# Performance work log

Hardware: AMD Instinct MI355X
Metric: run time of the kernel (lower is better)

## Reference

```python
import jax, jax.numpy as jnp
import numpy as np

EMB = 512
LIN = 64
ATT = 64
H = 8
EPS = 1e-6


def layer_norm(x, eps=EPS):
    # layer norm over last dim, no affine params (matches F.layer_norm w/o weight/bias)
    mu = jnp.mean(x, axis=-1, keepdims=True)
    var = jnp.var(x, axis=-1, keepdims=True)
    return (x - mu) * jax.lax.rsqrt(var + eps)


def setup_inputs() -> dict:
    key = jax.random.key(0)
    k1, k2, k3, k4, k5 = jax.random.split(key, 5)
    B, N = 8, 2048
    x = jax.random.normal(k1, (B, N, EMB), dtype=jnp.float32)
    rel_pos_bias = jax.random.normal(k2, (H, N, N), dtype=jnp.float32)
    invalid_attn_mask = jnp.ones((B, N, N), dtype=jnp.float32)
    uvqk = jax.random.normal(k3, (EMB, LIN * 2 * H + ATT * H * 2), dtype=jnp.float32) * 0.02
    o_w = jax.random.normal(k4, (EMB, LIN * H), dtype=jnp.float32) * (1.0 / np.sqrt(LIN * H))
    o_b = jnp.zeros((EMB,), dtype=jnp.float32)
    return {"x": x, "rel_pos_bias": rel_pos_bias, "invalid_attn_mask": invalid_attn_mask,
            "uvqk": uvqk, "o_w": o_w, "o_b": o_b}


def reference(x, rel_pos_bias, invalid_attn_mask, uvqk, o_w, o_b):
    B, N, D = x.shape
    residual = x
    normed = layer_norm(x)                                   # [B,N,D]
    proj = jax.nn.silu(jnp.einsum('bnd,de->bne', normed, uvqk))  # [B,N,2*LIN*H+2*ATT*H]
    lh = LIN * H
    ah = ATT * H
    u = proj[..., :lh]                                        # [B,N,LIN*H]
    v = proj[..., lh:2 * lh].reshape(B, N, H, LIN)            # [B,N,H,LIN]
    q = proj[..., 2 * lh:2 * lh + ah].reshape(B, N, H, ATT)
    k = proj[..., 2 * lh + ah:].reshape(B, N, H, ATT)
    qk = jnp.einsum('bnhd,bmhd->bhnm', q, k) + rel_pos_bias[None]  # [B,H,N,N]
    qk = jax.nn.silu(qk) * invalid_attn_mask[:, None]
    attn = jnp.einsum('bhnm,bmhd->bnhd', qk, v).reshape(B, N, lh)
    gated = u * layer_norm(attn)
    out = jnp.einsum('bnf,ef->bne', gated, o_w) + o_b          # dropout off (eval)
    return residual + out
```

## Files before the change

kernel.cpp:

```cpp
#include <hip/hip_runtime.h>
#include <stdint.h>

typedef short bf16x8   __attribute__((ext_vector_type(8)));
typedef short short4v  __attribute__((ext_vector_type(4)));
typedef short short8v  __attribute__((ext_vector_type(8)));
typedef float f32x4    __attribute__((ext_vector_type(4)));

typedef __attribute__((address_space(3))) uint32_t lds_u32;
typedef const __attribute__((address_space(1))) uint32_t glob_u32;

__device__ __forceinline__ void gl_lds16(const void* g, void* l) {
  __builtin_amdgcn_global_load_lds((glob_u32*)g, (lds_u32*)l, 16, 0, 0);
}

__device__ __forceinline__ float bf2f(short u) {
  union { float f; uint32_t i; } v; v.i = ((uint32_t)(uint16_t)u) << 16; return v.f;
}
__device__ __forceinline__ short f2bf(float f) {
  union { float f; uint32_t i; } v; v.f = f;
  uint32_t r = v.i + 0x7FFFu + ((v.i >> 16) & 1u);
  return (short)(r >> 16);
}
__device__ __forceinline__ float siluf(float x) {
  return x * __builtin_amdgcn_rcpf(1.0f + __expf(-x));
}
__device__ __forceinline__ f32x4 mfma16(bf16x8 a, bf16x8 b, f32x4 c) {
  return __builtin_amdgcn_mfma_f32_16x16x32_bf16(a, b, c, 0, 0, 0);
}
__device__ __forceinline__ uint32_t cvtpk_bf16(float lo, float hi) {
  uint32_t d;
  asm("v_cvt_pk_bf16_f32 %0, %1, %2" : "=v"(d) : "v"(lo), "v"(hi));
  return d;
}

__global__ __launch_bounds__(256) void k_ln(const float* __restrict__ x, short* __restrict__ xn) {
  int row = blockIdx.x * 4 + (threadIdx.x >> 6);
  int lane = threadIdx.x & 63;
  const float4* xr = (const float4*)(x + (size_t)row * 512);
  float4 a = xr[lane * 2], b = xr[lane * 2 + 1];
  float s  = a.x + a.y + a.z + a.w + b.x + b.y + b.z + b.w;
  float s2 = a.x*a.x + a.y*a.y + a.z*a.z + a.w*a.w + b.x*b.x + b.y*b.y + b.z*b.z + b.w*b.w;
#pragma unroll
  for (int m = 1; m < 64; m <<= 1) { s += __shfl_xor(s, m); s2 += __shfl_xor(s2, m); }
  float mu = s * (1.f / 512.f);
  float rstd = rsqrtf(s2 * (1.f / 512.f) - mu * mu + 1e-6f);
  float v[8] = {a.x, a.y, a.z, a.w, b.x, b.y, b.z, b.w};
  short8v o;
#pragma unroll
  for (int j = 0; j < 8; ++j) o[j] = f2bf((v[j] - mu) * rstd);
  *(short8v*)&xn[(size_t)row * 512 + lane * 8] = o;
}

__global__ __launch_bounds__(256) void k_prep_w(const float* __restrict__ uvqk, short* __restrict__ Wt) {
  __shared__ float t[64][65];
  int k0 = blockIdx.x * 64;
  int c0 = blockIdx.y * 64;
  for (int i = threadIdx.x; i < 64 * 64; i += 256) {
    int r = i >> 6, c = i & 63;
    t[r][c] = uvqk[(size_t)(k0 + r) * 2048 + c0 + c];
  }
  __syncthreads();
  for (int i = threadIdx.x; i < 64 * 64; i += 256) {
    int c = i >> 6, k = i & 63;
    Wt[(size_t)(c0 + c) * 512 + k0 + k] = f2bf(t[k][c]);
  }
}

__global__ __launch_bounds__(256) void k_cast_ow(const float* __restrict__ ow, short* __restrict__ owt) {
  int i = blockIdx.x * 256 + threadIdx.x;
  owt[i] = f2bf(ow[i]);
}

__device__ __forceinline__ void gemm_core(const short* __restrict__ A, const short* __restrict__ Bt,
                                          int t0, int c0, short* As, short* Bs, f32x4 (&acc)[4][4]) {
  int tid = threadIdx.x;
  int w = tid >> 6, lane = tid & 63, l16 = lane & 15, lq = lane >> 4;
  int wm = (w >> 1) * 64, wn = (w & 1) * 64;
  int srow = tid >> 3;
  int sch = (tid & 7) ^ (srow & 7);
  const short* ag = A  + (size_t)(t0 + srow) * 512 + sch * 8;
  const short* bg = Bt + (size_t)(c0 + srow) * 512 + sch * 8;

  for (int k0 = 0; k0 < 512; k0 += 64) {
#pragma unroll
    for (int j = 0; j < 4; ++j) {
      gl_lds16(ag + (size_t)j * 32 * 512 + k0, (char*)As + j * 4096 + w * 1024);
      gl_lds16(bg + (size_t)j * 32 * 512 + k0, (char*)Bs + j * 4096 + w * 1024);
    }
    asm volatile("s_waitcnt vmcnt(0)" ::: "memory");
    __syncthreads();
#pragma unroll
    for (int kk = 0; kk < 2; ++kk) {
      bf16x8 af[4], bf[4];
#pragma unroll
      for (int mi = 0; mi < 4; ++mi) {
        int row = wm + mi * 16 + l16;
        af[mi] = *(const bf16x8*)&As[row * 64 + (((kk * 4 + lq) ^ (l16 & 7)) * 8)];
      }
#pragma unroll
      for (int ni = 0; ni < 4; ++ni) {
        int row = wn + ni * 16 + l16;
        bf[ni] = *(const bf16x8*)&Bs[row * 64 + (((kk * 4 + lq) ^ (l16 & 7)) * 8)];
      }
#pragma unroll
      for (int mi = 0; mi < 4; ++mi)
#pragma unroll
        for (int ni = 0; ni < 4; ++ni)
          acc[mi][ni] = mfma16(af[mi], bf[ni], acc[mi][ni]);
    }
    __syncthreads();
  }
}

__global__ __launch_bounds__(256) void k_gemm1(const short* __restrict__ A, const short* __restrict__ Bt,
                                               short* __restrict__ proj, short* __restrict__ Vt) {
  __shared__ short As[128 * 64], Bs[128 * 64];
  int c0 = blockIdx.x * 128, t0 = blockIdx.y * 128;
  f32x4 acc[4][4] = {};
  gemm_core(A, Bt, t0, c0, As, Bs, acc);
  int tid = threadIdx.x, w = tid >> 6, lane = tid & 63, l16 = lane & 15, lq = lane >> 4;
  int wm = (w >> 1) * 64, wn = (w & 1) * 64;
  bool isv = (c0 >= 512 && c0 < 1024);
#pragma unroll
  for (int mi = 0; mi < 4; ++mi)
#pragma unroll
    for (int ni = 0; ni < 4; ++ni) {
      int c = c0 + wn + ni * 16 + l16;
      int trow = t0 + wm + mi * 16 + lq * 4;
      if (isv) {
        int hh = (c - 512) >> 6, d = (c - 512) & 63;
        int bb = trow >> 11, nn = trow & 2047;
        short4v pv;
#pragma unroll
        for (int i = 0; i < 4; ++i) pv[i] = f2bf(siluf(acc[mi][ni][i]));
        *(short4v*)&Vt[((size_t)(bb * 8 + hh) * 64 + d) * 2048 + nn] = pv;
      } else {
#pragma unroll
        for (int i = 0; i < 4; ++i)
          proj[(size_t)(trow + i) * 2048 + c] = f2bf(siluf(acc[mi][ni][i]));
      }
    }
}

__global__ __launch_bounds__(256, 4) void k_attn(const short* __restrict__ proj,
                                                 const short* __restrict__ Vt,
                                                 const float* __restrict__ rpb,
                                                 const float* __restrict__ maskp,
                                                 float* __restrict__ attn) {
  __shared__ __align__(16) short Ks[2][64 * 64];
  __shared__ __align__(16) short Vs[2][64 * 64];
  __shared__ __align__(16) short Ps[64 * 64];

  int p = blockIdx.x;
  int L = (p & 7) * 256 + (p >> 3);
  int qt = L >> 6, h = (L >> 3) & 7, b = L & 7;
  int n0 = qt * 64;

  int tid = threadIdx.x;
  int w = tid >> 6, lane = tid & 63, l16 = lane & 15, lq = lane >> 4;

  bf16x8 qf[2];
#pragma unroll
  for (int kk = 0; kk < 2; ++kk) {
    int n = n0 + w * 16 + l16;
    qf[kk] = *(const bf16x8*)&proj[(size_t)(b * 2048 + n) * 2048 + 1024 + h * 64 + kk * 32 + lq * 8];
  }

  int j8 = lane >> 3, c8 = lane & 7;
  int srcc = (c8 ^ j8) * 8;
  const short* kg = proj + (size_t)(b * 2048) * 2048 + 1536 + h * 64 + srcc;
  const short* vg = Vt + (size_t)((b * 8 + h) * 64) * 2048 + srcc;

  const float* rp_t = rpb   + (size_t)h * 4194304 + (size_t)(n0 + w * 16 + l16) * 2048 + lq * 4;
  const float* mk_t = maskp + (size_t)b * 4194304 + (size_t)(n0 + w * 16 + l16) * 2048 + lq * 4;

  f32x4 acc_o[4] = {};
  f32x4 rv[4], mv[4];

#pragma unroll
  for (int j = 0; j < 2; ++j) {
    gl_lds16(kg + (size_t)(w * 16 + j * 8 + j8) * 2048, &Ks[0][w * 1024 + j * 512]);
    gl_lds16(vg + (size_t)(w * 16 + j * 8 + j8) * 2048, &Vs[0][w * 1024 + j * 512]);
  }
  __builtin_amdgcn_sched_barrier(0);
#pragma unroll
  for (int ni = 0; ni < 4; ++ni) {
    rv[ni] = *(const f32x4*)(rp_t + ni * 16);
    mv[ni] = *(const f32x4*)(mk_t + ni * 16);
  }
  __builtin_amdgcn_sched_barrier(0);
  asm volatile("s_waitcnt vmcnt(8)" ::: "memory");
  __builtin_amdgcn_sched_barrier(0);
  __builtin_amdgcn_s_barrier();

  for (int t = 0; t < 32; ++t) {
    int kv0 = t << 6;
    const short* Kc = Ks[t & 1];
    const short* Vc = Vs[t & 1];

    if (t < 31) {
      short* Kn = Ks[(t & 1) ^ 1];
      short* Vn = Vs[(t & 1) ^ 1];
      int kvn = kv0 + 64;
#pragma unroll
      for (int j = 0; j < 2; ++j) {
        gl_lds16(kg + (size_t)(kvn + w * 16 + j * 8 + j8) * 2048, &Kn[w * 1024 + j * 512]);
        gl_lds16(vg + (size_t)(w * 16 + j * 8 + j8) * 2048 + kvn, &Vn[w * 1024 + j * 512]);
      }
    }
    __builtin_amdgcn_sched_barrier(0);

    f32x4 s[4];
#pragma unroll
    for (int ni = 0; ni < 4; ++ni) s[ni] = (f32x4){0.f, 0.f, 0.f, 0.f};
    __builtin_amdgcn_s_setprio(1);
#pragma unroll
    for (int kk = 0; kk < 2; ++kk) {
      bf16x8 kf[4];
#pragma unroll
      for (int ni = 0; ni < 4; ++ni)
        kf[ni] = *(const bf16x8*)&Kc[(ni * 16 + l16) * 64 + (((kk * 4 + lq) ^ (l16 & 7)) * 8)];
#pragma unroll
      for (int ni = 0; ni < 4; ++ni)
        s[ni] = mfma16(kf[ni], qf[kk], s[ni]);
    }
    __builtin_amdgcn_s_setprio(0);

    {
      int row = w * 16 + l16;
      char* pr = (char*)Ps + row * 128;
      int swz = (l16 & 7) << 4;
#pragma unroll
      for (int ni = 0; ni < 4; ++ni) {
        float pv[4];
#pragma unroll
        for (int i = 0; i < 4; ++i) {
          float xx = s[ni][i] + rv[ni][i];
          pv[i] = siluf(xx) * mv[ni][i];
        }
        union { uint32_t u[2]; short4v sv; } pk;
        pk.u[0] = cvtpk_bf16(pv[0], pv[1]);
        pk.u[1] = cvtpk_bf16(pv[2], pv[3]);
        *(short4v*)(pr + ((ni * 32 + lq * 8) ^ swz)) = pk.sv;
      }
    }

    __builtin_amdgcn_s_setprio(1);
#pragma unroll
    for (int ks = 0; ks < 2; ++ks) {
      bf16x8 pf, vf[4];
      {
        int rp = w * 16 + l16;
        pf = *(const bf16x8*)((const char*)Ps + rp * 128 + (((ks * 4 + lq) << 4) ^ ((l16 & 7) << 4)));
      }
#pragma unroll
      for (int ni = 0; ni < 4; ++ni)
        vf[ni] = *(const bf16x8*)&Vc[(ni * 16 + l16) * 64 + (((ks * 4 + lq) ^ (l16 & 7)) * 8)];
#pragma unroll
      for (int ni = 0; ni < 4; ++ni)
        acc_o[ni] = mfma16(pf, vf[ni], acc_o[ni]);
    }
    __builtin_amdgcn_s_setprio(0);

    __builtin_amdgcn_sched_barrier(0);
    {
      int kvp = (t < 31) ? kv0 + 64 : kv0;
#pragma unroll
      for (int ni = 0; ni < 4; ++ni) {
        rv[ni] = *(const f32x4*)(rp_t + kvp + ni * 16);
        mv[ni] = *(const f32x4*)(mk_t + kvp + ni * 16);
      }
    }
    __builtin_amdgcn_sched_barrier(0);
    asm volatile("s_waitcnt vmcnt(8)" ::: "memory");
    __builtin_amdgcn_sched_barrier(0);
    __builtin_amdgcn_s_barrier();
  }

#pragma unroll
  for (int ni = 0; ni < 4; ++ni)
#pragma unroll
    for (int i = 0; i < 4; ++i) {
      int n = n0 + w * 16 + lq * 4 + i;
      attn[(size_t)(b * 2048 + n) * 512 + h * 64 + ni * 16 + l16] = acc_o[ni][i];
    }
}

__global__ __launch_bounds__(256) void k_gate(const float* __restrict__ attn, const short* __restrict__ proj,
                                              short* __restrict__ gated) {
  int row = blockIdx.x * 4 + (threadIdx.x >> 6);
  int lane = threadIdx.x & 63;
  const float4* ar = (const float4*)(attn + (size_t)row * 512);
  float4 a = ar[lane * 2], b = ar[lane * 2 + 1];
  float s  = a.x + a.y + a.z + a.w + b.x + b.y + b.z + b.w;
  float s2 = a.x*a.x + a.y*a.y + a.z*a.z + a.w*a.w + b.x*b.x + b.y*b.y + b.z*b.z + b.w*b.w;
#pragma unroll
  for (int m = 1; m < 64; m <<= 1) { s += __shfl_xor(s, m); s2 += __shfl_xor(s2, m); }
  float mu = s * (1.f / 512.f);
  float rstd = rsqrtf(s2 * (1.f / 512.f) - mu * mu + 1e-6f);
  float v[8] = {a.x, a.y, a.z, a.w, b.x, b.y, b.z, b.w};
  short8v u = *(const short8v*)&proj[(size_t)row * 2048 + lane * 8];
  short8v g;
#pragma unroll
  for (int j = 0; j < 8; ++j) g[j] = f2bf(bf2f(u[j]) * ((v[j] - mu) * rstd));
  *(short8v*)&gated[(size_t)row * 512 + lane * 8] = g;
}

__global__ __launch_bounds__(256) void k_gemm2(const short* __restrict__ A, const short* __restrict__ Bt,
                                               const float* __restrict__ ob, const float* __restrict__ x,
                                               float* __restrict__ out) {
  __shared__ short As[128 * 64], Bs[128 * 64];
  int c0 = blockIdx.x * 128, t0 = blockIdx.y * 128;
  f32x4 acc[4][4] = {};
  gemm_core(A, Bt, t0, c0, As, Bs, acc);
  int tid = threadIdx.x, w = tid >> 6, lane = tid & 63, l16 = lane & 15, lq = lane >> 4;
  int wm = (w >> 1) * 64, wn = (w & 1) * 64;
#pragma unroll
  for (int mi = 0; mi < 4; ++mi)
#pragma unroll
    for (int ni = 0; ni < 4; ++ni) {
      int e = c0 + wn + ni * 16 + l16;
      float bias = ob[e];
#pragma unroll
      for (int i = 0; i < 4; ++i) {
        int t = t0 + wm + mi * 16 + lq * 4 + i;
        out[(size_t)t * 512 + e] = acc[mi][ni][i] + bias + x[(size_t)t * 512 + e];
      }
    }
}

extern "C" void kernel_launch(void* const* d_in, const int* in_sizes, int n_in,
                              void* d_out, int out_size, void* d_ws, size_t ws_size,
                              hipStream_t stream) {
  const float* x    = (const float*)d_in[0];
  const float* rpb  = (const float*)d_in[1];
  const float* mask = (const float*)d_in[2];
  const float* uvqk = (const float*)d_in[3];
  const float* o_w  = (const float*)d_in[4];
  const float* o_b  = (const float*)d_in[5];
  float* out = (float*)d_out;

  char* p = (char*)d_ws;
  short* xn   = (short*)p; p += 16384ull * 512 * 2;
  short* Wt   = (short*)p; p += 2048ull * 512 * 2;
  short* owt  = (short*)p; p += 512ull * 512 * 2;
  short* proj = (short*)p; p += 16384ull * 2048 * 2;
  short* Vt   = (short*)p; p += 8ull * 8 * 64 * 2048 * 2;
  float* attn = (float*)p; p += 16384ull * 512 * 4;
  short* gated = xn;

  k_ln    <<<4096, 256, 0, stream>>>(x, xn);
  k_prep_w<<<dim3(8, 32), 256, 0, stream>>>(uvqk, Wt);
  k_cast_ow<<<1024, 256, 0, stream>>>(o_w, owt);
  k_gemm1 <<<dim3(16, 128), 256, 0, stream>>>(xn, Wt, proj, Vt);
  k_attn  <<<2048, 256, 0, stream>>>(proj, Vt, rpb, mask, attn);
  k_gate  <<<4096, 256, 0, stream>>>(attn, proj, gated);
  k_gemm2 <<<dim3(4, 128), 256, 0, stream>>>(gated, owt, o_b, x, out);
}
```

Baseline: 412.8 us.

## Convert rel-pos bias to bf16 and skip mask loads when mask is all ones

A new prep kernel converts rel_pos_bias to bf16 in workspace and scans the mask, clearing a flag if any element differs from 1. The attention kernel then reads the half-width bias and skips the per-head mask loads entirely when the flag says the mask is all ones. It also remaps block indices so the query tile varies fastest. The aim is to cut the repeated fp32 streaming of bias and mask, which dominates attention traffic. The cost is an extra full pass over bias and mask each call, and bf16 rounding of the bias.

```diff
diff --git a/kernel.cpp b/kernel.cpp
--- a/kernel.cpp
+++ b/kernel.cpp
@@ -51,7 +51,9 @@
   *(short8v*)&xn[(size_t)row * 512 + lane * 8] = o;
 }
 
-__global__ __launch_bounds__(256) void k_prep_w(const float* __restrict__ uvqk, short* __restrict__ Wt) {
+__global__ __launch_bounds__(256) void k_prep_w(const float* __restrict__ uvqk, short* __restrict__ Wt,
+                                                int* __restrict__ flag) {
+  if (blockIdx.x == 0 && blockIdx.y == 0 && threadIdx.x == 0) *flag = 1;
   __shared__ float t[64][65];
   int k0 = blockIdx.x * 64;
   int c0 = blockIdx.y * 64;
@@ -69,6 +71,25 @@
 __global__ __launch_bounds__(256) void k_cast_ow(const float* __restrict__ ow, short* __restrict__ owt) {
   int i = blockIdx.x * 256 + threadIdx.x;
   owt[i] = f2bf(ow[i]);
+}
+
+__global__ __launch_bounds__(256) void k_prep_rm(const float* __restrict__ rpb, const float* __restrict__ mask,
+                                                 short* __restrict__ rpbh, int* __restrict__ flag) {
+  bool ok = true;
+  for (int i = blockIdx.x * 256 + threadIdx.x; i < 4194304; i += 2048 * 256) {
+    const float4* r4 = (const float4*)rpb + (size_t)i * 2;
+    float4 a = r4[0], b = r4[1];
+    float v[8] = {a.x, a.y, a.z, a.w, b.x, b.y, b.z, b.w};
+    short8v o;
+#pragma unroll
+    for (int j = 0; j < 8; ++j) o[j] = f2bf(v[j]);
+    *(short8v*)&rpbh[(size_t)i * 8] = o;
+    const float4* m4 = (const float4*)mask + (size_t)i * 2;
+    float4 ma = m4[0], mb = m4[1];
+    ok = ok && (ma.x == 1.f) && (ma.y == 1.f) && (ma.z == 1.f) && (ma.w == 1.f)
+            && (mb.x == 1.f) && (mb.y == 1.f) && (mb.z == 1.f) && (mb.w == 1.f);
+  }
+  if (!ok) *flag = 0;
 }
 
 __device__ __forceinline__ void gemm_core(const short* __restrict__ A, const short* __restrict__ Bt,
@@ -142,10 +163,12 @@
     }
 }
 
+template<bool BF>
 __global__ __launch_bounds__(256, 4) void k_attn(const short* __restrict__ proj,
                                                  const short* __restrict__ Vt,
-                                                 const float* __restrict__ rpb,
+                                                 const void* __restrict__ rpbp,
                                                  const float* __restrict__ maskp,
+                                                 const int* __restrict__ flag,
                                                  float* __restrict__ attn) {
   __shared__ __align__(16) short Ks[2][64 * 64];
   __shared__ __align__(16) short Vs[2][64 * 64];
@@ -153,11 +176,15 @@
 
   int p = blockIdx.x;
   int L = (p & 7) * 256 + (p >> 3);
-  int qt = L >> 6, h = (L >> 3) & 7, b = L & 7;
+  int qt = L & 31, hb = L >> 5;
+  int h = hb >> 3, b = hb & 7;
   int n0 = qt * 64;
 
   int tid = threadIdx.x;
   int w = tid >> 6, lane = tid & 63, l16 = lane & 15, lq = lane >> 4;
+
+  bool use_mask = true;
+  if (BF) use_mask = (*flag == 0);
 
   bf16x8 qf[2];
 #pragma unroll
@@ -171,11 +198,17 @@
   const short* kg = proj + (size_t)(b * 2048) * 2048 + 1536 + h * 64 + srcc;
   const short* vg = Vt + (size_t)((b * 8 + h) * 64) * 2048 + srcc;
 
-  const float* rp_t = rpb   + (size_t)h * 4194304 + (size_t)(n0 + w * 16 + l16) * 2048 + lq * 4;
+  size_t rmoff = (size_t)h * 4194304 + (size_t)(n0 + w * 16 + l16) * 2048 + lq * 4;
+  const short* rp_h = (const short*)rpbp + rmoff;
+  const float* rp_f = (const float*)rpbp + rmoff;
   const float* mk_t = maskp + (size_t)b * 4194304 + (size_t)(n0 + w * 16 + l16) * 2048 + lq * 4;
 
   f32x4 acc_o[4] = {};
-  f32x4 rv[4], mv[4];
+  short4v rvh[4];
+  f32x4   rvf[4];
+  f32x4   mv[4];
+#pragma unroll
+  for (int ni = 0; ni < 4; ++ni) mv[ni] = (f32x4){1.f, 1.f, 1.f, 1.f};
 
 #pragma unroll
   for (int j = 0; j < 2; ++j) {
@@ -185,11 +218,16 @@
   __builtin_amdgcn_sched_barrier(0);
 #pragma unroll
   for (int ni = 0; ni < 4; ++ni) {
-    rv[ni] = *(const f32x4*)(rp_t + ni * 16);
-    mv[ni] = *(const f32x4*)(mk_t + ni * 16);
+    if (BF) rvh[ni] = *(const short4v*)(rp_h + ni * 16);
+    else    rvf[ni] = *(const f32x4*)(rp_f + ni * 16);
+  }
+  if (use_mask) {
+#pragma unroll
+    for (int ni = 0; ni < 4; ++ni) mv[ni] = *(const f32x4*)(mk_t + ni * 16);
   }
   __builtin_amdgcn_sched_barrier(0);
-  asm volatile("s_waitcnt vmcnt(8)" ::: "memory");
+  if (use_mask) asm volatile("s_waitcnt vmcnt(8)" ::: "memory");
+  else          asm volatile("s_waitcnt vmcnt(4)" ::: "memory");
   __builtin_amdgcn_sched_barrier(0);
   __builtin_amdgcn_s_barrier();
 
@@ -235,7 +273,8 @@
         float pv[4];
 #pragma unroll
         for (int i = 0; i < 4; ++i) {
-          float xx = s[ni][i] + rv[ni][i];
+          float r = BF ? bf2f(rvh[ni][i]) : rvf[ni][i];
+          float xx = s[ni][i] + r;
           pv[i] = siluf(xx) * mv[ni][i];
         }
         union { uint32_t u[2]; short4v sv; } pk;
@@ -267,12 +306,17 @@
       int kvp = (t < 31) ? kv0 + 64 : kv0;
 #pragma unroll
       for (int ni = 0; ni < 4; ++ni) {
-        rv[ni] = *(const f32x4*)(rp_t + kvp + ni * 16);
-        mv[ni] = *(const f32x4*)(mk_t + kvp + ni * 16);
+        if (BF) rvh[ni] = *(const short4v*)(rp_h + kvp + ni * 16);
+        else    rvf[ni] = *(const f32x4*)(rp_f + kvp + ni * 16);
+      }
+      if (use_mask) {
+#pragma unroll
+        for (int ni = 0; ni < 4; ++ni) mv[ni] = *(const f32x4*)(mk_t + kvp + ni * 16);
       }
     }
     __builtin_amdgcn_sched_barrier(0);
-    asm volatile("s_waitcnt vmcnt(8)" ::: "memory");
+    if (use_mask) asm volatile("s_waitcnt vmcnt(8)" ::: "memory");
+    else          asm volatile("s_waitcnt vmcnt(4)" ::: "memory");
     __builtin_amdgcn_sched_barrier(0);
     __builtin_amdgcn_s_barrier();
   }
@@ -347,13 +391,22 @@
   short* proj = (short*)p; p += 16384ull * 2048 * 2;
   short* Vt   = (short*)p; p += 8ull * 8 * 64 * 2048 * 2;
   float* attn = (float*)p; p += 16384ull * 512 * 4;
+  short* rpbh = (short*)p; p += 33554432ull * 2;
+  int*   flag = (int*)p;   p += 256;
   short* gated = xn;
 
+  bool bf_ok = ws_size >= (size_t)(p - (char*)d_ws);
+
   k_ln    <<<4096, 256, 0, stream>>>(x, xn);
-  k_prep_w<<<dim3(8, 32), 256, 0, stream>>>(uvqk, Wt);
+  k_prep_w<<<dim3(8, 32), 256, 0, stream>>>(uvqk, Wt, bf_ok ? flag : (int*)attn);
   k_cast_ow<<<1024, 256, 0, stream>>>(o_w, owt);
+  if (bf_ok)
+    k_prep_rm<<<2048, 256, 0, stream>>>(rpb, mask, rpbh, flag);
   k_gemm1 <<<dim3(16, 128), 256, 0, stream>>>(xn, Wt, proj, Vt);
-  k_attn  <<<2048, 256, 0, stream>>>(proj, Vt, rpb, mask, attn);
+  if (bf_ok)
+    k_attn<true> <<<2048, 256, 0, stream>>>(proj, Vt, rpbh, mask, flag, attn);
+  else
+    k_attn<false><<<2048, 256, 0, stream>>>(proj, Vt, rpb, mask, (const int*)attn, attn);
   k_gate  <<<4096, 256, 0, stream>>>(attn, proj, gated);
   k_gemm2 <<<dim3(4, 128), 256, 0, stream>>>(gated, owt, o_b, x, out);
 }
```

After: 369.0 us. 1.12x faster.
